# Performance work log

Hardware: AMD Instinct MI355X
Metric: run time of the kernel (lower is better)

## Reference

```python
import jax, jax.numpy as jnp
import numpy as np


def setup_inputs() -> dict:
    key = jax.random.key(0)
    ks = jax.random.split(key, 8)
    B, N, F = 16, 2048, 128
    x = jax.random.normal(ks[0], (B, N, F), dtype=jnp.float32)
    # dense (pre-normalized) adjacency, as spektral GCNConv expects normalized A
    a = jax.random.uniform(ks[1], (B, N, N), dtype=jnp.float32) / N
    w1 = jax.random.normal(ks[2], (F, 32), dtype=jnp.float32) * 0.1
    b1 = jnp.zeros((32,), dtype=jnp.float32)
    w2 = jax.random.normal(ks[3], (32, 32), dtype=jnp.float32) * 0.1
    b2 = jnp.zeros((32,), dtype=jnp.float32)
    wf1 = jax.random.normal(ks[4], (32, 512), dtype=jnp.float32) * 0.1
    bf1 = jnp.zeros((512,), dtype=jnp.float32)
    wf2 = jax.random.normal(ks[5], (512, 1), dtype=jnp.float32) * 0.1
    bf2 = jnp.zeros((1,), dtype=jnp.float32)
    return {"x": x, "a": a, "w1": w1, "b1": b1, "w2": w2, "b2": b2,
            "wf1": wf1, "bf1": bf1, "wf2": wf2, "bf2": bf2}


def _gcn(x, a, w, b):
    # GCNConv: elu(A_norm @ X @ W + b)
    h = jnp.einsum('bnf,fc->bnc', x, w)   # dense transform first (cheaper)
    h = jnp.einsum('bnm,bmc->bnc', a, h)  # adjacency aggregation
    return jax.nn.elu(h + b)


def reference(x, a, w1, b1, w2, b2, wf1, bf1, wf2, bf2):
    h = _gcn(x, a, w1, b1)                # [B,N,32]
    h = _gcn(h, a, w2, b2)                # [B,N,32]
    pooled = jnp.sum(h, axis=1)           # GlobalSumPool -> [B,32]
    h = jax.nn.relu(pooled @ wf1 + bf1)   # [B,512]
    out = jax.nn.sigmoid(h @ wf2 + bf2)   # [B,1]
    return out
```

## Files before the change

### kernel.cpp

```cpp
#include <hip/hip_runtime.h>
#include <hip/hip_bf16.h>
#include <math.h>

#define BATCH 16
#define NN 2048
#define FF 128
#define CC 32
#define HID 512

typedef float v4f __attribute__((ext_vector_type(4)));
typedef short short8 __attribute__((ext_vector_type(8)));

__device__ __forceinline__ unsigned short f2bf(float f) {
  unsigned u = __float_as_uint(f);
  u += 0x7fffu + ((u >> 16) & 1u);
  return (unsigned short)(u >> 16);
}

__device__ __forceinline__ float elu1(float x) {
  return x > 0.f ? x : expm1f(x);
}

template<int K, bool SRC_BF16>
__global__ __launch_bounds__(256)
void k_xw(const void* __restrict__ src, const float* __restrict__ w,
          unsigned short* __restrict__ outT) {
  int t = threadIdx.x;
  int wv = t >> 6, l = t & 63, lo = l & 15, q = l >> 4;
  int rowt = blockIdx.x * 4 + wv;
  long row = (long)rowt * 16 + lo;

  short8 wf[K / 32][2];
#pragma unroll
  for (int kc = 0; kc < K / 32; ++kc)
#pragma unroll
    for (int h = 0; h < 2; ++h) {
      short8 f;
#pragma unroll
      for (int j = 0; j < 8; ++j)
        f[j] = (short)f2bf(w[(kc * 32 + q * 8 + j) * CC + h * 16 + lo]);
      wf[kc][h] = f;
    }

  v4f acc0 = {0.f, 0.f, 0.f, 0.f}, acc1 = {0.f, 0.f, 0.f, 0.f};
#pragma unroll
  for (int kc = 0; kc < K / 32; ++kc) {
    short8 af;
    if constexpr (SRC_BF16) {
      const unsigned short* sp = (const unsigned short*)src + row * K + kc * 32 + q * 8;
      af = *(const short8*)sp;
    } else {
      const float* sp = (const float*)src + row * K + kc * 32 + q * 8;
      float4 a0 = *(const float4*)sp;
      float4 a1 = *(const float4*)(sp + 4);
      af[0] = (short)f2bf(a0.x); af[1] = (short)f2bf(a0.y);
      af[2] = (short)f2bf(a0.z); af[3] = (short)f2bf(a0.w);
      af[4] = (short)f2bf(a1.x); af[5] = (short)f2bf(a1.y);
      af[6] = (short)f2bf(a1.z); af[7] = (short)f2bf(a1.w);
    }
    acc0 = __builtin_amdgcn_mfma_f32_16x16x32_bf16(af, wf[kc][0], acc0, 0, 0, 0);
    acc1 = __builtin_amdgcn_mfma_f32_16x16x32_bf16(af, wf[kc][1], acc1, 0, 0, 0);
  }

  int b = rowt >> 7;
  int nbase = (rowt & 127) * 16;
#pragma unroll
  for (int r = 0; r < 4; ++r) {
    int n = nbase + q * 4 + r;
    outT[((long)b * CC + lo) * NN + n] = f2bf(acc0[r]);
    outT[((long)b * CC + 16 + lo) * NN + n] = f2bf(acc1[r]);
  }
}

#define SM 512
#define LDS_STRIDE 520

__global__ __launch_bounds__(256)
void k_agg(const float* __restrict__ a,
           const unsigned short* __restrict__ hT,
           const float* __restrict__ bias,
           unsigned short* __restrict__ h_out,
           float* __restrict__ pooled,
           int mode) {
  __shared__ unsigned short hs[CC * LDS_STRIDE];

  int t = threadIdx.x;
  int b = blockIdx.x >> 5;
  int rt = blockIdx.x & 31;
  int wv = t >> 6, l = t & 63, lo = l & 15, q = l >> 4;
  int n_wave = rt * 64 + wv * 16;

  const float* arow = a + ((long)(b * NN + n_wave + lo)) * NN;

  v4f acc0 = {0.f, 0.f, 0.f, 0.f}, acc1 = {0.f, 0.f, 0.f, 0.f};

  for (int ms = 0; ms < NN; ms += SM) {
    __syncthreads();
    for (int i = t; i < CC * (SM / 8); i += 256) {
      int c = i >> 6;
      int qd = i & 63;
      uint4 v = *(const uint4*)(hT + ((long)b * CC + c) * NN + ms + qd * 8);
      *(uint4*)&hs[c * LDS_STRIDE + qd * 8] = v;
    }
    __syncthreads();

#pragma unroll 4
    for (int mm = 0; mm < SM; mm += 32) {
      int mg = ms + mm + q * 8;
      float4 a0 = *(const float4*)(arow + mg);
      float4 a1 = *(const float4*)(arow + mg + 4);
      short8 af;
      af[0] = (short)f2bf(a0.x); af[1] = (short)f2bf(a0.y);
      af[2] = (short)f2bf(a0.z); af[3] = (short)f2bf(a0.w);
      af[4] = (short)f2bf(a1.x); af[5] = (short)f2bf(a1.y);
      af[6] = (short)f2bf(a1.z); af[7] = (short)f2bf(a1.w);
      short8 b0 = *(const short8*)&hs[lo * LDS_STRIDE + mm + q * 8];
      short8 b1 = *(const short8*)&hs[(16 + lo) * LDS_STRIDE + mm + q * 8];
      acc0 = __builtin_amdgcn_mfma_f32_16x16x32_bf16(af, b0, acc0, 0, 0, 0);
      acc1 = __builtin_amdgcn_mfma_f32_16x16x32_bf16(af, b1, acc1, 0, 0, 0);
    }
  }

  if (mode == 0) {
#pragma unroll
    for (int r = 0; r < 4; ++r) {
      int n = n_wave + q * 4 + r;
      float v0 = elu1(acc0[r] + bias[lo]);
      float v1 = elu1(acc1[r] + bias[16 + lo]);
      h_out[((long)(b * NN + n)) * CC + lo] = f2bf(v0);
      h_out[((long)(b * NN + n)) * CC + 16 + lo] = f2bf(v1);
    }
  } else {
    float p0 = 0.f, p1 = 0.f;
#pragma unroll
    for (int r = 0; r < 4; ++r) {
      p0 += elu1(acc0[r] + bias[lo]);
      p1 += elu1(acc1[r] + bias[16 + lo]);
    }
    p0 += __shfl_xor(p0, 16, 64);
    p0 += __shfl_xor(p0, 32, 64);
    p1 += __shfl_xor(p1, 16, 64);
    p1 += __shfl_xor(p1, 32, 64);
    if (q == 0) {
      atomicAdd(&pooled[b * CC + lo], p0);
      atomicAdd(&pooled[b * CC + 16 + lo], p1);
    }
  }
}

__global__ __launch_bounds__(512)
void k5_mlp(const float* __restrict__ pooled, const float* __restrict__ wf1,
            const float* __restrict__ bf1, const float* __restrict__ wf2,
            const float* __restrict__ bf2, float* __restrict__ out) {
  __shared__ float red[HID];
  __shared__ float ps[CC];
  int b = blockIdx.x, j = threadIdx.x;
  if (j < CC) ps[j] = pooled[b * CC + j];
  __syncthreads();
  float acc = bf1[j];
#pragma unroll
  for (int c = 0; c < CC; ++c) acc += ps[c] * wf1[c * HID + j];
  red[j] = fmaxf(acc, 0.f) * wf2[j];
  __syncthreads();
  for (int s = HID / 2; s > 0; s >>= 1) {
    if (j < s) red[j] += red[j + s];
    __syncthreads();
  }
  if (j == 0) out[b] = 1.f / (1.f + expf(-(red[0] + bf2[0])));
}

extern "C" void kernel_launch(void* const* d_in, const int* in_sizes, int n_in,
                              void* d_out, int out_size, void* d_ws, size_t ws_size,
                              hipStream_t stream) {
  const float* x   = (const float*)d_in[0];
  const float* a   = (const float*)d_in[1];
  const float* w1  = (const float*)d_in[2];
  const float* b1  = (const float*)d_in[3];
  const float* w2  = (const float*)d_in[4];
  const float* b2  = (const float*)d_in[5];
  const float* wf1 = (const float*)d_in[6];
  const float* bf1 = (const float*)d_in[7];
  const float* wf2 = (const float*)d_in[8];
  const float* bf2 = (const float*)d_in[9];
  float* out = (float*)d_out;

  char* ws = (char*)d_ws;
  unsigned short* hT1 = (unsigned short*)ws;
  unsigned short* h1  = (unsigned short*)(ws + (2 << 20));
  unsigned short* hT2 = (unsigned short*)ws;
  float* pooled = (float*)(ws + (4 << 20));

  hipMemsetAsync(pooled, 0, BATCH * CC * sizeof(float), stream);

  k_xw<FF, false><<<512, 256, 0, stream>>>((const void*)x, w1, hT1);
  k_agg<<<BATCH * (NN / 64), 256, 0, stream>>>(a, hT1, b1, h1, nullptr, 0);
  k_xw<CC, true><<<512, 256, 0, stream>>>((const void*)h1, w2, hT2);
  k_agg<<<BATCH * (NN / 64), 256, 0, stream>>>(a, hT2, b2, nullptr, pooled, 1);
  k5_mlp<<<BATCH, HID, 0, stream>>>(pooled, wf1, bf1, wf2, bf2, out);
}
```

Baseline: 466.2 us.

## Split aggregation K dimension across two wave halves, drop LDS staging of H

The aggregation kernel now uses 512 threads, with two groups of waves each covering half of the node (K) dimension and reading H directly from global memory instead of staging it in LDS with barriers. The partial accumulators are combined through LDS, after which bias, ELU and a packed 64-bit bf16 store are applied. Pooling is reduced in LDS before one global atomic per channel. The aim is more memory-level parallelism on the bandwidth-bound read of A and fewer block-wide syncs, at the cost of redundant global H reads and an extra LDS reduction.

Result: no change. 469.5 us (+0.7%).

```diff
diff --git a/kernel.cpp b/kernel.cpp
--- a/kernel.cpp
+++ b/kernel.cpp
@@ -72,80 +72,76 @@
   }
 }
 
-#define SM 512
-#define LDS_STRIDE 520
+#define MH 1024
 
-__global__ __launch_bounds__(256)
+__global__ __launch_bounds__(512, 4)
 void k_agg(const float* __restrict__ a,
            const unsigned short* __restrict__ hT,
            const float* __restrict__ bias,
            unsigned short* __restrict__ h_out,
            float* __restrict__ pooled,
            int mode) {
-  __shared__ unsigned short hs[CC * LDS_STRIDE];
+  __shared__ float lacc[2][64][33];
+  __shared__ float lpool[CC];
 
   int t = threadIdx.x;
   int b = blockIdx.x >> 5;
   int rt = blockIdx.x & 31;
-  int wv = t >> 6, l = t & 63, lo = l & 15, q = l >> 4;
-  int n_wave = rt * 64 + wv * 16;
+  int wv = t >> 6;
+  int tile = wv & 3, half = wv >> 2;
+  int l = t & 63, lo = l & 15, q = l >> 4;
+  int n0 = rt * 64 + tile * 16;
 
-  const float* arow = a + ((long)(b * NN + n_wave + lo)) * NN;
+  const float* arow = a + ((long)(b * NN + n0 + lo)) * NN + half * MH;
+  const unsigned short* hrow0 = hT + ((long)b * CC + lo) * NN + half * MH;
+  const unsigned short* hrow1 = hT + ((long)b * CC + 16 + lo) * NN + half * MH;
 
   v4f acc0 = {0.f, 0.f, 0.f, 0.f}, acc1 = {0.f, 0.f, 0.f, 0.f};
 
-  for (int ms = 0; ms < NN; ms += SM) {
-    __syncthreads();
-    for (int i = t; i < CC * (SM / 8); i += 256) {
-      int c = i >> 6;
-      int qd = i & 63;
-      uint4 v = *(const uint4*)(hT + ((long)b * CC + c) * NN + ms + qd * 8);
-      *(uint4*)&hs[c * LDS_STRIDE + qd * 8] = v;
-    }
-    __syncthreads();
-
 #pragma unroll 4
-    for (int mm = 0; mm < SM; mm += 32) {
-      int mg = ms + mm + q * 8;
-      float4 a0 = *(const float4*)(arow + mg);
-      float4 a1 = *(const float4*)(arow + mg + 4);
-      short8 af;
-      af[0] = (short)f2bf(a0.x); af[1] = (short)f2bf(a0.y);
-      af[2] = (short)f2bf(a0.z); af[3] = (short)f2bf(a0.w);
-      af[4] = (short)f2bf(a1.x); af[5] = (short)f2bf(a1.y);
-      af[6] = (short)f2bf(a1.z); af[7] = (short)f2bf(a1.w);
-      short8 b0 = *(const short8*)&hs[lo * LDS_STRIDE + mm + q * 8];
-      short8 b1 = *(const short8*)&hs[(16 + lo) * LDS_STRIDE + mm + q * 8];
-      acc0 = __builtin_amdgcn_mfma_f32_16x16x32_bf16(af, b0, acc0, 0, 0, 0);
-      acc1 = __builtin_amdgcn_mfma_f32_16x16x32_bf16(af, b1, acc1, 0, 0, 0);
-    }
+  for (int mm = 0; mm < MH; mm += 32) {
+    int off = mm + q * 8;
+    float4 a0 = *(const float4*)(arow + off);
+    float4 a1 = *(const float4*)(arow + off + 4);
+    short8 bf0 = *(const short8*)(hrow0 + off);
+    short8 bf1 = *(const short8*)(hrow1 + off);
+    short8 af;
+    af[0] = (short)f2bf(a0.x); af[1] = (short)f2bf(a0.y);
+    af[2] = (short)f2bf(a0.z); af[3] = (short)f2bf(a0.w);
+    af[4] = (short)f2bf(a1.x); af[5] = (short)f2bf(a1.y);
+    af[6] = (short)f2bf(a1.z); af[7] = (short)f2bf(a1.w);
+    acc0 = __builtin_amdgcn_mfma_f32_16x16x32_bf16(af, bf0, acc0, 0, 0, 0);
+    acc1 = __builtin_amdgcn_mfma_f32_16x16x32_bf16(af, bf1, acc1, 0, 0, 0);
   }
 
+#pragma unroll
+  for (int r = 0; r < 4; ++r) {
+    int nl = tile * 16 + q * 4 + r;
+    lacc[half][nl][lo] = acc0[r];
+    lacc[half][nl][16 + lo] = acc1[r];
+  }
+  if (t < CC) lpool[t] = 0.f;
+  __syncthreads();
+
+  int nl = t >> 3, cb = (t & 7) * 4;
+  float v[4];
+#pragma unroll
+  for (int j = 0; j < 4; ++j)
+    v[j] = elu1(lacc[0][nl][cb + j] + lacc[1][nl][cb + j] + bias[cb + j]);
+
   if (mode == 0) {
+    unsigned long long pk =
+        (unsigned long long)f2bf(v[0]) |
+        ((unsigned long long)f2bf(v[1]) << 16) |
+        ((unsigned long long)f2bf(v[2]) << 32) |
+        ((unsigned long long)f2bf(v[3]) << 48);
+    *(unsigned long long*)&h_out[((long)(b * NN + rt * 64 + nl)) * CC + cb] = pk;
+  } else {
 #pragma unroll
-    for (int r = 0; r < 4; ++r) {
-      int n = n_wave + q * 4 + r;
-      float v0 = elu1(acc0[r] + bias[lo]);
-      float v1 = elu1(acc1[r] + bias[16 + lo]);
-      h_out[((long)(b * NN + n)) * CC + lo] = f2bf(v0);
-      h_out[((long)(b * NN + n)) * CC + 16 + lo] = f2bf(v1);
-    }
-  } else {
-    float p0 = 0.f, p1 = 0.f;
-#pragma unroll
-    for (int r = 0; r < 4; ++r) {
-      p0 += elu1(acc0[r] + bias[lo]);
-      p1 += elu1(acc1[r] + bias[16 + lo]);
-    }
-    p0 += __shfl_xor(p0, 16, 64);
-    p0 += __shfl_xor(p0, 32, 64);
-    p1 += __shfl_xor(p1, 16, 64);
-    p1 += __shfl_xor(p1, 32, 64);
-    if (q == 0) {
-      atomicAdd(&pooled[b * CC + lo], p0);
-      atomicAdd(&pooled[b * CC + 16 + lo], p1);
-    }
+    for (int j = 0; j < 4; ++j) atomicAdd(&lpool[cb + j], v[j]);
   }
+  __syncthreads();
+  if (mode == 1 && t < CC) atomicAdd(&pooled[b * CC + t], lpool[t]);
 }
 
 __global__ __launch_bounds__(512)
@@ -193,8 +189,8 @@
   hipMemsetAsync(pooled, 0, BATCH * CC * sizeof(float), stream);
 
   k_xw<FF, false><<<512, 256, 0, stream>>>((const void*)x, w1, hT1);
-  k_agg<<<BATCH * (NN / 64), 256, 0, stream>>>(a, hT1, b1, h1, nullptr, 0);
+  k_agg<<<BATCH * (NN / 64), 512, 0, stream>>>(a, hT1, b1, h1, nullptr, 0);
   k_xw<CC, true><<<512, 256, 0, stream>>>((const void*)h1, w2, hT2);
-  k_agg<<<BATCH * (NN / 64), 256, 0, stream>>>(a, hT2, b2, nullptr, pooled, 1);
+  k_agg<<<BATCH * (NN / 64), 512, 0, stream>>>(a, hT2, b2, nullptr, pooled, 1);
   k5_mlp<<<BATCH, HID, 0, stream>>>(pooled, wf1, bf1, wf2, bf2, out);
 }
```

## Pre-convert adjacency to bf16 once and split aggregation K across two blocks

Applied to the files above, without the earlier changes.

A new kernel converts the fp32 adjacency to bf16 once per call, so both aggregation passes stream half-size bf16 rows and skip the in-loop conversion. Aggregation is split into two K-halves, which doubles the grid and stages each half of hT in LDS with a single sync. The halves write fp32 partials, and the bias plus ELU epilogue moves into the next transform (k_xw2) or a new pooling kernel. This costs an extra full read and write of A for the conversion, extra partial-buffer traffic and one more launch, in exchange for better occupancy and lighter agg passes.

After: 483.8 us. 1.04x slower.

```diff
diff --git a/kernel.cpp b/kernel.cpp
--- a/kernel.cpp
+++ b/kernel.cpp
@@ -21,18 +21,34 @@
   return x > 0.f ? x : expm1f(x);
 }
 
-template<int K, bool SRC_BF16>
-__global__ __launch_bounds__(256)
-void k_xw(const void* __restrict__ src, const float* __restrict__ w,
-          unsigned short* __restrict__ outT) {
+__global__ __launch_bounds__(256)
+void k_cvt(const float* __restrict__ a, unsigned short* __restrict__ abf) {
+  long base = ((long)blockIdx.x * 256 + threadIdx.x) * 32;
+  float4 f[8];
+#pragma unroll
+  for (int i = 0; i < 8; ++i) f[i] = *(const float4*)(a + base + i * 4);
+#pragma unroll
+  for (int i = 0; i < 4; ++i) {
+    short8 r;
+    r[0] = (short)f2bf(f[2 * i].x);     r[1] = (short)f2bf(f[2 * i].y);
+    r[2] = (short)f2bf(f[2 * i].z);     r[3] = (short)f2bf(f[2 * i].w);
+    r[4] = (short)f2bf(f[2 * i + 1].x); r[5] = (short)f2bf(f[2 * i + 1].y);
+    r[6] = (short)f2bf(f[2 * i + 1].z); r[7] = (short)f2bf(f[2 * i + 1].w);
+    *(short8*)(abf + base + i * 8) = r;
+  }
+}
+
+__global__ __launch_bounds__(256)
+void k_xw1(const float* __restrict__ src, const float* __restrict__ w,
+           unsigned short* __restrict__ outT) {
   int t = threadIdx.x;
   int wv = t >> 6, l = t & 63, lo = l & 15, q = l >> 4;
   int rowt = blockIdx.x * 4 + wv;
   long row = (long)rowt * 16 + lo;
 
-  short8 wf[K / 32][2];
-#pragma unroll
-  for (int kc = 0; kc < K / 32; ++kc)
+  short8 wf[FF / 32][2];
+#pragma unroll
+  for (int kc = 0; kc < FF / 32; ++kc)
 #pragma unroll
     for (int h = 0; h < 2; ++h) {
       short8 f;
@@ -44,20 +60,15 @@
 
   v4f acc0 = {0.f, 0.f, 0.f, 0.f}, acc1 = {0.f, 0.f, 0.f, 0.f};
 #pragma unroll
-  for (int kc = 0; kc < K / 32; ++kc) {
+  for (int kc = 0; kc < FF / 32; ++kc) {
+    const float* sp = src + row * FF + kc * 32 + q * 8;
+    float4 a0 = *(const float4*)sp;
+    float4 a1 = *(const float4*)(sp + 4);
     short8 af;
-    if constexpr (SRC_BF16) {
-      const unsigned short* sp = (const unsigned short*)src + row * K + kc * 32 + q * 8;
-      af = *(const short8*)sp;
-    } else {
-      const float* sp = (const float*)src + row * K + kc * 32 + q * 8;
-      float4 a0 = *(const float4*)sp;
-      float4 a1 = *(const float4*)(sp + 4);
-      af[0] = (short)f2bf(a0.x); af[1] = (short)f2bf(a0.y);
-      af[2] = (short)f2bf(a0.z); af[3] = (short)f2bf(a0.w);
-      af[4] = (short)f2bf(a1.x); af[5] = (short)f2bf(a1.y);
-      af[6] = (short)f2bf(a1.z); af[7] = (short)f2bf(a1.w);
-    }
+    af[0] = (short)f2bf(a0.x); af[1] = (short)f2bf(a0.y);
+    af[2] = (short)f2bf(a0.z); af[3] = (short)f2bf(a0.w);
+    af[4] = (short)f2bf(a1.x); af[5] = (short)f2bf(a1.y);
+    af[6] = (short)f2bf(a1.z); af[7] = (short)f2bf(a1.w);
     acc0 = __builtin_amdgcn_mfma_f32_16x16x32_bf16(af, wf[kc][0], acc0, 0, 0, 0);
     acc1 = __builtin_amdgcn_mfma_f32_16x16x32_bf16(af, wf[kc][1], acc1, 0, 0, 0);
   }
@@ -72,80 +83,125 @@
   }
 }
 
-#define SM 512
-#define LDS_STRIDE 520
-
-__global__ __launch_bounds__(256)
-void k_agg(const float* __restrict__ a,
+__global__ __launch_bounds__(256)
+void k_xw2(const float* __restrict__ h1f, const float* __restrict__ b1,
+           const float* __restrict__ w2, unsigned short* __restrict__ outT) {
+  const long HALF = (long)BATCH * NN * CC;
+  int t = threadIdx.x;
+  int wv = t >> 6, l = t & 63, lo = l & 15, q = l >> 4;
+  int rowt = blockIdx.x * 4 + wv;
+  long row = (long)rowt * 16 + lo;
+
+  short8 wf[2];
+#pragma unroll
+  for (int h = 0; h < 2; ++h) {
+    short8 f;
+#pragma unroll
+    for (int j = 0; j < 8; ++j)
+      f[j] = (short)f2bf(w2[(q * 8 + j) * CC + h * 16 + lo]);
+    wf[h] = f;
+  }
+
+  const float* p0 = h1f + row * CC + q * 8;
+  const float* p1 = p0 + HALF;
+  float4 x0 = *(const float4*)p0;
+  float4 x1 = *(const float4*)(p0 + 4);
+  float4 y0 = *(const float4*)p1;
+  float4 y1 = *(const float4*)(p1 + 4);
+  float bb[8];
+#pragma unroll
+  for (int j = 0; j < 8; ++j) bb[j] = b1[q * 8 + j];
+  short8 af;
+  af[0] = (short)f2bf(elu1(x0.x + y0.x + bb[0]));
+  af[1] = (short)f2bf(elu1(x0.y + y0.y + bb[1]));
+  af[2] = (short)f2bf(elu1(x0.z + y0.z + bb[2]));
+  af[3] = (short)f2bf(elu1(x0.w + y0.w + bb[3]));
+  af[4] = (short)f2bf(elu1(x1.x + y1.x + bb[4]));
+  af[5] = (short)f2bf(elu1(x1.y + y1.y + bb[5]));
+  af[6] = (short)f2bf(elu1(x1.z + y1.z + bb[6]));
+  af[7] = (short)f2bf(elu1(x1.w + y1.w + bb[7]));
+
+  v4f acc0 = {0.f, 0.f, 0.f, 0.f}, acc1 = {0.f, 0.f, 0.f, 0.f};
+  acc0 = __builtin_amdgcn_mfma_f32_16x16x32_bf16(af, wf[0], acc0, 0, 0, 0);
+  acc1 = __builtin_amdgcn_mfma_f32_16x16x32_bf16(af, wf[1], acc1, 0, 0, 0);
+
+  int b = rowt >> 7;
+  int nbase = (rowt & 127) * 16;
+#pragma unroll
+  for (int r = 0; r < 4; ++r) {
+    int n = nbase + q * 4 + r;
+    outT[((long)b * CC + lo) * NN + n] = f2bf(acc0[r]);
+    outT[((long)b * CC + 16 + lo) * NN + n] = f2bf(acc1[r]);
+  }
+}
+
+#define LSTR 1032
+
+__global__ __launch_bounds__(256, 2)
+void k_agg(const unsigned short* __restrict__ abf,
            const unsigned short* __restrict__ hT,
-           const float* __restrict__ bias,
-           unsigned short* __restrict__ h_out,
-           float* __restrict__ pooled,
-           int mode) {
-  __shared__ unsigned short hs[CC * LDS_STRIDE];
-
-  int t = threadIdx.x;
-  int b = blockIdx.x >> 5;
-  int rt = blockIdx.x & 31;
+           float* __restrict__ hpart) {
+  __shared__ unsigned short hs[CC * LSTR];
+
+  int t = threadIdx.x;
+  int bid = blockIdx.x;
+  int rt = bid & 31, half = (bid >> 5) & 1, b = bid >> 6;
+
+#pragma unroll
+  for (int i = 0; i < 16; ++i) {
+    int j = i * 256 + t;
+    int c = j >> 7, off = (j & 127) * 8;
+    uint4 v = *(const uint4*)(hT + ((long)b * CC + c) * NN + half * 1024 + off);
+    *(uint4*)&hs[c * LSTR + off] = v;
+  }
+  __syncthreads();
+
   int wv = t >> 6, l = t & 63, lo = l & 15, q = l >> 4;
-  int n_wave = rt * 64 + wv * 16;
-
-  const float* arow = a + ((long)(b * NN + n_wave + lo)) * NN;
+  int n0 = rt * 64 + wv * 16;
+  const unsigned short* arow =
+      abf + ((long)(b * NN + n0 + lo)) * NN + half * 1024 + q * 8;
+  const unsigned short* h0 = &hs[lo * LSTR + q * 8];
 
   v4f acc0 = {0.f, 0.f, 0.f, 0.f}, acc1 = {0.f, 0.f, 0.f, 0.f};
-
-  for (int ms = 0; ms < NN; ms += SM) {
-    __syncthreads();
-    for (int i = t; i < CC * (SM / 8); i += 256) {
-      int c = i >> 6;
-      int qd = i & 63;
-      uint4 v = *(const uint4*)(hT + ((long)b * CC + c) * NN + ms + qd * 8);
-      *(uint4*)&hs[c * LDS_STRIDE + qd * 8] = v;
-    }
-    __syncthreads();
-
-#pragma unroll 4
-    for (int mm = 0; mm < SM; mm += 32) {
-      int mg = ms + mm + q * 8;
-      float4 a0 = *(const float4*)(arow + mg);
-      float4 a1 = *(const float4*)(arow + mg + 4);
-      short8 af;
-      af[0] = (short)f2bf(a0.x); af[1] = (short)f2bf(a0.y);
-      af[2] = (short)f2bf(a0.z); af[3] = (short)f2bf(a0.w);
-      af[4] = (short)f2bf(a1.x); af[5] = (short)f2bf(a1.y);
-      af[6] = (short)f2bf(a1.z); af[7] = (short)f2bf(a1.w);
-      short8 b0 = *(const short8*)&hs[lo * LDS_STRIDE + mm + q * 8];
-      short8 b1 = *(const short8*)&hs[(16 + lo) * LDS_STRIDE + mm + q * 8];
-      acc0 = __builtin_amdgcn_mfma_f32_16x16x32_bf16(af, b0, acc0, 0, 0, 0);
-      acc1 = __builtin_amdgcn_mfma_f32_16x16x32_bf16(af, b1, acc1, 0, 0, 0);
-    }
-  }
-
-  if (mode == 0) {
-#pragma unroll
-    for (int r = 0; r < 4; ++r) {
-      int n = n_wave + q * 4 + r;
-      float v0 = elu1(acc0[r] + bias[lo]);
-      float v1 = elu1(acc1[r] + bias[16 + lo]);
-      h_out[((long)(b * NN + n)) * CC + lo] = f2bf(v0);
-      h_out[((long)(b * NN + n)) * CC + 16 + lo] = f2bf(v1);
-    }
-  } else {
-    float p0 = 0.f, p1 = 0.f;
-#pragma unroll
-    for (int r = 0; r < 4; ++r) {
-      p0 += elu1(acc0[r] + bias[lo]);
-      p1 += elu1(acc1[r] + bias[16 + lo]);
-    }
-    p0 += __shfl_xor(p0, 16, 64);
-    p0 += __shfl_xor(p0, 32, 64);
-    p1 += __shfl_xor(p1, 16, 64);
-    p1 += __shfl_xor(p1, 32, 64);
-    if (q == 0) {
-      atomicAdd(&pooled[b * CC + lo], p0);
-      atomicAdd(&pooled[b * CC + 16 + lo], p1);
-    }
-  }
+#pragma unroll
+  for (int mm = 0; mm < 1024; mm += 32) {
+    short8 af = *(const short8*)(arow + mm);
+    short8 b0 = *(const short8*)(h0 + mm);
+    short8 b1 = *(const short8*)(h0 + 16 * LSTR + mm);
+    acc0 = __builtin_amdgcn_mfma_f32_16x16x32_bf16(af, b0, acc0, 0, 0, 0);
+    acc1 = __builtin_amdgcn_mfma_f32_16x16x32_bf16(af, b1, acc1, 0, 0, 0);
+  }
+
+  float* op = hpart + ((long)half * BATCH * NN + (long)b * NN) * CC;
+#pragma unroll
+  for (int r = 0; r < 4; ++r) {
+    int n = n0 + q * 4 + r;
+    op[(long)n * CC + lo] = acc0[r];
+    op[(long)n * CC + 16 + lo] = acc1[r];
+  }
+}
+
+__global__ __launch_bounds__(256)
+void k_pool(const float* __restrict__ h2f, const float* __restrict__ b2,
+            float* __restrict__ pooled) {
+  const long HALF = (long)BATCH * NN * CC;
+  __shared__ float red[8][CC + 1];
+  int t = threadIdx.x;
+  int b = blockIdx.x >> 3, seg = blockIdx.x & 7;
+  int c = t & 31, nl = t >> 5;
+  float bc = b2[c];
+  float s = 0.f;
+  for (int n = seg * 256 + nl; n < seg * 256 + 256; n += 8) {
+    long idx = ((long)b * NN + n) * CC + c;
+    s += elu1(h2f[idx] + h2f[HALF + idx] + bc);
+  }
+  red[nl][c] = s;
+  __syncthreads();
+  if (nl < 4) red[nl][c] += red[nl + 4][c];
+  __syncthreads();
+  if (nl < 2) red[nl][c] += red[nl + 2][c];
+  __syncthreads();
+  if (nl == 0) atomicAdd(&pooled[b * CC + c], red[0][c] + red[1][c]);
 }
 
 __global__ __launch_bounds__(512)
@@ -185,16 +241,20 @@
   float* out = (float*)d_out;
 
   char* ws = (char*)d_ws;
-  unsigned short* hT1 = (unsigned short*)ws;
-  unsigned short* h1  = (unsigned short*)(ws + (2 << 20));
-  unsigned short* hT2 = (unsigned short*)ws;
-  float* pooled = (float*)(ws + (4 << 20));
+  unsigned short* abf = (unsigned short*)ws;
+  unsigned short* hT1 = (unsigned short*)(ws + 0x8000000UL);
+  unsigned short* hT2 = (unsigned short*)(ws + 0x8200000UL);
+  float* h1f = (float*)(ws + 0x8400000UL);
+  float* h2f = (float*)(ws + 0x8C00000UL);
+  float* pooled = (float*)(ws + 0x9400000UL);
 
   hipMemsetAsync(pooled, 0, BATCH * CC * sizeof(float), stream);
 
-  k_xw<FF, false><<<512, 256, 0, stream>>>((const void*)x, w1, hT1);
-  k_agg<<<BATCH * (NN / 64), 256, 0, stream>>>(a, hT1, b1, h1, nullptr, 0);
-  k_xw<CC, true><<<512, 256, 0, stream>>>((const void*)h1, w2, hT2);
-  k_agg<<<BATCH * (NN / 64), 256, 0, stream>>>(a, hT2, b2, nullptr, pooled, 1);
+  k_cvt<<<8192, 256, 0, stream>>>(a, abf);
+  k_xw1<<<512, 256, 0, stream>>>(x, w1, hT1);
+  k_agg<<<1024, 256, 0, stream>>>(abf, hT1, h1f);
+  k_xw2<<<512, 256, 0, stream>>>(h1f, b1, w2, hT2);
+  k_agg<<<1024, 256, 0, stream>>>(abf, hT2, h2f);
+  k_pool<<<128, 256, 0, stream>>>(h2f, b2, pooled);
   k5_mlp<<<BATCH, HID, 0, stream>>>(pooled, wf1, bf1, wf2, bf2, out);
 }
```
